# Kernel tuning notes

Hardware: AMD Instinct MI355X
Metric: run time of the kernel (lower is better)

Reference implementation:

```python
import jax, jax.numpy as jnp
import numpy as np

N_NODES = 50000
N_EDGES = 800000
D_IN = 64
D_OUT = 64
N_REL = 8


def setup_inputs() -> dict:
    key = jax.random.key(0)
    ks = jax.random.split(key, 7)
    x = jax.random.normal(ks[0], (N_NODES, D_IN), jnp.float32)
    src = jax.random.randint(ks[1], (N_EDGES,), 0, N_NODES)   # neighbor ids
    dst = jax.random.randint(ks[2], (N_EDGES,), 0, N_NODES)   # center node ids
    rel = jax.random.randint(ks[3], (N_EDGES,), 0, N_REL)
    # xavier_uniform for W_r: [R, 2*d, d]
    lim = float(np.sqrt(6.0 / (2 * D_IN + D_IN)))
    W_r = jax.random.uniform(ks[4], (N_REL, 2 * D_IN, D_IN), jnp.float32, -lim, lim)
    # nn.Linear(2*d, d_out): weight [d_out, 2*d], bias [d_out]
    lim2 = float(1.0 / np.sqrt(2 * D_IN))
    W_lin = jax.random.uniform(ks[5], (D_OUT, 2 * D_IN), jnp.float32, -lim2, lim2)
    b_lin = jax.random.uniform(ks[6], (D_OUT,), jnp.float32, -lim2, lim2)
    return {"x": x, "src": src, "dst": dst, "rel": rel,
            "W_r": W_r, "W_lin": W_lin, "b_lin": b_lin}


def reference(x, src, dst, rel, W_r, W_lin, b_lin):
    n, d = x.shape
    e = src.shape[0]
    # gate logit per edge: (concat(x[dst], x[src]) @ W_r[rel]).sum(-1)
    # == concat(x[dst], x[src]) . W_r[rel].sum(-1)  -- mathematically identical,
    # avoids materializing the [E, 2d, d] matmul the torch loop performs.
    w = W_r.sum(-1)                      # [R, 2d]
    w_dst, w_src = w[:, :d], w[:, d:]    # [R, d] each
    logit = jnp.sum(x[dst] * w_dst[rel], axis=-1) + jnp.sum(x[src] * w_src[rel], axis=-1)  # [E]
    gate = jax.nn.sigmoid(logit)[:, None]        # [E, 1]
    weighted = x[src] * gate                     # [E, d]
    # scatter-mean over destination nodes (nodes with no edges stay zero)
    agg_sum = jax.ops.segment_sum(weighted, dst, num_segments=n)            # [N, d]
    cnt = jax.ops.segment_sum(jnp.ones((e,), x.dtype), dst, num_segments=n)  # [N]
    agg = agg_sum / jnp.maximum(cnt, 1.0)[:, None]
    combined = jnp.concatenate([x, agg], axis=-1)  # [N, 2d]
    out = combined @ W_lin.T + b_lin               # [N, d_out]
    return jax.nn.leaky_relu(out, negative_slope=0.01)
```

## Files before the change

### kernel.cpp

```cpp
#include <hip/hip_runtime.h>
#include <hip/hip_fp16.h>
#include <cmath>

#define N_NODES 50000
#define N_EDGES 800000
#define D 64
#define N_REL 8

#define NODES_PER_BLK 32
#define TN 16
#define MAXDEG 64
#define NSEG 8
#define SEG_DIV 6250

static __device__ __forceinline__ unsigned f2bf(float f) {
    unsigned u = __float_as_uint(f);
    return (u + 0x7FFFu + ((u >> 16) & 1u)) >> 16;
}
#define BFLO(u) __uint_as_float((u) << 16)
#define BFHI(u) __uint_as_float((u) & 0xFFFF0000u)

__global__ void wprep_kernel(const float* __restrict__ W_r, float* __restrict__ w,
                             int* __restrict__ cnt) {
    int t = blockIdx.x * blockDim.x + threadIdx.x;
    if (t < N_REL * 2 * D) {
        const float* p = W_r + (size_t)t * D;
        float s = 0.0f;
#pragma unroll
        for (int k = 0; k < D; ++k) s += p[k];
        w[t] = s;
    }
    for (int i = t; i < N_NODES; i += gridDim.x * blockDim.x)
        cnt[i] = 0;
}

__global__ __launch_bounds__(256) void tables_kernel(
    const float* __restrict__ x, const float* __restrict__ w,
    float* __restrict__ Dn, float* __restrict__ Sr,
    unsigned short* __restrict__ xb)
{
    __shared__ float xs[TN][68];
    __shared__ float ws[16][68];

    int tid = threadIdx.x;
    int n0  = blockIdx.x * TN;

    for (int i = tid; i < 16 * 64; i += 256)
        ws[i >> 6][i & 63] = w[i];
    for (int i = tid; i < TN * 64; i += 256) {
        int n = n0 + (i >> 6);
        xs[i >> 6][i & 63] = (n < N_NODES) ? x[(size_t)n * D + (i & 63)] : 0.f;
    }
    __syncthreads();

    for (int i = tid; i < TN * 64; i += 256) {
        int n = n0 + (i >> 6);
        if (n < N_NODES) xb[(size_t)n0 * D + i] = (unsigned short)f2bf(xs[i >> 6][i & 63]);
    }

    int q = tid & 15, nl = tid >> 4;
    float acc = 0.f;
#pragma unroll
    for (int k = 0; k < 64; k += 4) {
        float4 a = *(const float4*)&xs[nl][k];
        float4 b = *(const float4*)&ws[q][k];
        acc += a.x * b.x + a.y * b.y + a.z * b.z + a.w * b.w;
    }
    int n = n0 + nl;
    if (n < N_NODES) {
        int r = q >> 1;
        if ((q & 1) == 0) Dn[n * 8 + r] = acc;
        else              Sr[n * 8 + r] = acc;
    }
}

__global__ __launch_bounds__(256) void scatter_kernel(
    const int* __restrict__ src, const int* __restrict__ dst,
    const int* __restrict__ rel,
    int* __restrict__ cnt,
    const float* __restrict__ Dn, const float* __restrict__ Sr,
    unsigned int* __restrict__ epack) {
    int seg   = blockIdx.x & (NSEG - 1);
    int chunk = blockIdx.x >> 3;
    int e = chunk * 256 + threadIdx.x;
    if (e >= N_EDGES) return;

    int d = dst[e];
    int s = src[e];
    int r = rel[e];
    asm volatile("" :: "v"(d), "v"(s), "v"(r));

    if ((unsigned)d / SEG_DIV != (unsigned)seg) return;

    int rank = atomicAdd(&cnt[d], 1);

    float logit = Dn[d * 8 + r] + Sr[s * 8 + r];
    float gate = 1.0f / (1.0f + __expf(-logit));
    if (rank < MAXDEG) {
        unsigned pv = ((unsigned)__half_as_ushort(__float2half_rn(gate)) << 16)
                    | (unsigned)s;
        epack[(size_t)d * MAXDEG + rank] = pv;
    }
}

__global__ __launch_bounds__(256) void agg_kernel(
    const unsigned short* __restrict__ xb,
    const int*   __restrict__ cnt,
    const unsigned int* __restrict__ epack,
    unsigned int* __restrict__ aggb)
{
    int n    = (blockIdx.x * blockDim.x + threadIdx.x) >> 6;
    int lane = threadIdx.x & 63;
    if (n >= N_NODES) return;

    int deg = cnt[n];
    int m   = (deg < MAXDEG) ? deg : MAXDEG;

    unsigned ev = 0u;
    if (lane < m) ev = epack[(size_t)n * MAXDEG + lane];
    float gl = __half2float(__ushort_as_half((unsigned short)(ev >> 16)));
    int   ol = (int)(ev & 0xFFFFu) * D;

    int sub = lane >> 4;
    int q4  = (lane & 15) * 4;

    float ax = 0.f, ay = 0.f, az = 0.f, aw = 0.f;

    for (int base = 0; base < m; base += 8) {
        int e0 = base + sub;
        int e1 = base + 4 + sub;
        float g0 = __shfl(gl, e0, 64);
        int   o0 = __shfl(ol, e0, 64);
        float g1 = __shfl(gl, e1, 64);
        int   o1 = __shfl(ol, e1, 64);
        uint2 u0 = *(const uint2*)&xb[(size_t)o0 + q4];
        uint2 u1 = *(const uint2*)&xb[(size_t)o1 + q4];
        ax += g0 * BFLO(u0.x) + g1 * BFLO(u1.x);
        ay += g0 * BFHI(u0.x) + g1 * BFHI(u1.x);
        az += g0 * BFLO(u0.y) + g1 * BFLO(u1.y);
        aw += g0 * BFHI(u0.y) + g1 * BFHI(u1.y);
    }

#pragma unroll
    for (int off = 16; off <= 32; off <<= 1) {
        ax += __shfl_xor(ax, off, 64);
        ay += __shfl_xor(ay, off, 64);
        az += __shfl_xor(az, off, 64);
        aw += __shfl_xor(aw, off, 64);
    }

    if (sub == 0) {
        float inv = 1.0f / fmaxf((float)deg, 1.0f);
        uint2 pr;
        pr.x = f2bf(ax * inv) | (f2bf(ay * inv) << 16);
        pr.y = f2bf(az * inv) | (f2bf(aw * inv) << 16);
        *(uint2*)&aggb[(size_t)n * 32 + 2 * (lane & 15)] = pr;
    }
}

__global__ __launch_bounds__(256, 6) void lin_kernel(
    const unsigned int* __restrict__ xbu,
    const unsigned int* __restrict__ aggb,
    const float* __restrict__ W_lin,
    const float* __restrict__ b_lin,
    float* __restrict__ out)
{
    __shared__ unsigned int W2[64][66];
    __shared__ unsigned int c2[NODES_PER_BLK][66];
    __shared__ float b_lds[64];

    int tid = threadIdx.x;
    int n0  = blockIdx.x * NODES_PER_BLK;

    for (int i = tid; i < 64 * 64; i += 256) {
        int j = i >> 6, kp = i & 63;
        float2 wv = *(const float2*)&W_lin[j * 128 + kp * 2];
        W2[j][kp] = f2bf(wv.x) | (f2bf(wv.y) << 16);
    }
    if (tid < 64) b_lds[tid] = b_lin[tid];

    for (int i = tid; i < NODES_PER_BLK * 32; i += 256) {
        int nl = i >> 5, kp = i & 31;
        int n  = n0 + nl;
        unsigned vx = 0u, va = 0u;
        if (n < N_NODES) {
            vx = xbu[(size_t)n * 32 + kp];
            va = aggb[(size_t)n * 32 + kp];
        }
        c2[nl][kp]      = vx;
        c2[nl][32 + kp] = va;
    }
    __syncthreads();

    int tx = tid & 15, ty = tid >> 4;
    float acc[2][4];
#pragma unroll
    for (int i = 0; i < 2; ++i)
#pragma unroll
        for (int jj = 0; jj < 4; ++jj) acc[i][jj] = b_lds[tx + 16 * jj];

#pragma unroll 2
    for (int kp = 0; kp < 64; kp += 2) {
        uint2 cu[2], wu[4];
        cu[0] = *(const uint2*)&c2[ty][kp];
        cu[1] = *(const uint2*)&c2[ty + 16][kp];
#pragma unroll
        for (int jj = 0; jj < 4; ++jj)
            wu[jj] = *(const uint2*)&W2[tx + 16 * jj][kp];
#pragma unroll
        for (int i = 0; i < 2; ++i) {
            float cx = BFLO(cu[i].x), cy = BFHI(cu[i].x);
            float cz = BFLO(cu[i].y), cw = BFHI(cu[i].y);
#pragma unroll
            for (int jj = 0; jj < 4; ++jj) {
                acc[i][jj] += cx * BFLO(wu[jj].x) + cy * BFHI(wu[jj].x)
                            + cz * BFLO(wu[jj].y) + cw * BFHI(wu[jj].y);
            }
        }
    }

#pragma unroll
    for (int i = 0; i < 2; ++i) {
        int n = n0 + ty + 16 * i;
        if (n < N_NODES) {
#pragma unroll
            for (int jj = 0; jj < 4; ++jj) {
                float v = acc[i][jj];
                out[(size_t)n * D + tx + 16 * jj] = (v > 0.f) ? v : 0.01f * v;
            }
        }
    }
}

extern "C" void kernel_launch(void* const* d_in, const int* in_sizes, int n_in,
                              void* d_out, int out_size, void* d_ws, size_t ws_size,
                              hipStream_t stream) {
    const float* x     = (const float*)d_in[0];
    const int*   src   = (const int*)  d_in[1];
    const int*   dst   = (const int*)  d_in[2];
    const int*   rel   = (const int*)  d_in[3];
    const float* W_r   = (const float*)d_in[4];
    const float* W_lin = (const float*)d_in[5];
    const float* b_lin = (const float*)d_in[6];
    float* out = (float*)d_out;

    char* p = (char*)d_ws;
    float*  w       = (float*)p;                p += 4096;
    float*  Dn      = (float*)p;                p += (size_t)N_NODES * 8 * 4;
    float*  Sr      = (float*)p;                p += (size_t)N_NODES * 8 * 4;
    int*    cnt     = (int*)p;                  p += 256 * 1024;
    unsigned int* epack = (unsigned int*)p;     p += (size_t)N_NODES * MAXDEG * 4;
    unsigned short* xb = (unsigned short*)p;    p += (size_t)N_NODES * D * 2;
    unsigned int* aggb = (unsigned int*)p;      p += (size_t)N_NODES * 32 * 4;

    wprep_kernel<<<512, 256, 0, stream>>>(W_r, w, cnt);
    tables_kernel<<<(N_NODES + TN - 1) / TN, 256, 0, stream>>>(x, w, Dn, Sr, xb);
    scatter_kernel<<<NSEG * ((N_EDGES + 255) / 256), 256, 0, stream>>>(
        src, dst, rel, cnt, Dn, Sr, epack);
    agg_kernel<<<(N_NODES * 64 + 255) / 256, 256, 0, stream>>>(xb, cnt, epack, aggb);
    lin_kernel<<<(N_NODES + NODES_PER_BLK - 1) / NODES_PER_BLK, 256, 0, stream>>>(
        (const unsigned int*)xb, aggb, W_lin, b_lin, out);
}
```

Measured before the change: 176.3 us.

## Split scatter into gate pass plus segment-bucketed compaction and placement pass

```diff
diff --git a/kernel.cpp b/kernel.cpp
--- a/kernel.cpp
+++ b/kernel.cpp
@@ -12,6 +12,7 @@
 #define MAXDEG 64
 #define NSEG 8
 #define SEG_DIV 6250
+#define SEG_STRIDE 112640
 
 static __device__ __forceinline__ unsigned f2bf(float f) {
     unsigned u = __float_as_uint(f);
@@ -21,7 +22,7 @@
 #define BFHI(u) __uint_as_float((u) & 0xFFFF0000u)
 
 __global__ void wprep_kernel(const float* __restrict__ W_r, float* __restrict__ w,
-                             int* __restrict__ cnt) {
+                             int* __restrict__ cnt, int* __restrict__ segCnt) {
     int t = blockIdx.x * blockDim.x + threadIdx.x;
     if (t < N_REL * 2 * D) {
         const float* p = W_r + (size_t)t * D;
@@ -30,6 +31,7 @@
         for (int k = 0; k < D; ++k) s += p[k];
         w[t] = s;
     }
+    if (t < 128) segCnt[t] = 0;
     for (int i = t; i < N_NODES; i += gridDim.x * blockDim.x)
         cnt[i] = 0;
 }
@@ -74,33 +76,60 @@
     }
 }
 
-__global__ __launch_bounds__(256) void scatter_kernel(
+__global__ __launch_bounds__(256) void gate_kernel(
     const int* __restrict__ src, const int* __restrict__ dst,
     const int* __restrict__ rel,
-    int* __restrict__ cnt,
+    int* __restrict__ cnt, int* __restrict__ segCnt,
     const float* __restrict__ Dn, const float* __restrict__ Sr,
-    unsigned int* __restrict__ epack) {
-    int seg   = blockIdx.x & (NSEG - 1);
-    int chunk = blockIdx.x >> 3;
-    int e = chunk * 256 + threadIdx.x;
-    if (e >= N_EDGES) return;
+    uint2* __restrict__ compact)
+{
+    int e    = blockIdx.x * 256 + threadIdx.x;
+    int lane = threadIdx.x & 63;
 
     int d = dst[e];
     int s = src[e];
     int r = rel[e];
     asm volatile("" :: "v"(d), "v"(s), "v"(r));
 
-    if ((unsigned)d / SEG_DIV != (unsigned)seg) return;
-
     int rank = atomicAdd(&cnt[d], 1);
 
     float logit = Dn[d * 8 + r] + Sr[s * 8 + r];
     float gate = 1.0f / (1.0f + __expf(-logit));
-    if (rank < MAXDEG) {
-        unsigned pv = ((unsigned)__half_as_ushort(__float2half_rn(gate)) << 16)
-                    | (unsigned)s;
-        epack[(size_t)d * MAXDEG + rank] = pv;
-    }
+
+    uint2 rec;
+    rec.x = ((unsigned)__half_as_ushort(__float2half_rn(gate)) << 16) | (unsigned)s;
+    rec.y = ((unsigned)rank << 16) | (unsigned)d;
+
+    unsigned seg = (unsigned)d / SEG_DIV;
+
+#pragma unroll
+    for (int k = 0; k < NSEG; ++k) {
+        unsigned long long m = __ballot(seg == (unsigned)k);
+        if (seg == (unsigned)k) {
+            int pop    = __popcll(m);
+            int before = __popcll(m & ((1ull << lane) - 1ull));
+            int leader = (int)__ffsll((long long)m) - 1;
+            int base = 0;
+            if (lane == leader) base = atomicAdd(&segCnt[k * 16], pop);
+            base = __shfl(base, leader, 64);
+            compact[(size_t)k * SEG_STRIDE + base + before] = rec;
+        }
+    }
+}
+
+__global__ __launch_bounds__(256) void place_kernel(
+    const int* __restrict__ segCnt, const uint2* __restrict__ compact,
+    unsigned int* __restrict__ epack)
+{
+    int seg   = blockIdx.x & (NSEG - 1);
+    int chunk = blockIdx.x >> 3;
+    int i = chunk * 256 + threadIdx.x;
+    if (i >= segCnt[seg * 16]) return;
+    uint2 rec = compact[(size_t)seg * SEG_STRIDE + i];
+    int d    = (int)(rec.y & 0xFFFFu);
+    int rank = (int)(rec.y >> 16);
+    if (rank < MAXDEG)
+        epack[(size_t)d * MAXDEG + rank] = rec.x;
 }
 
 __global__ __launch_bounds__(256) void agg_kernel(
@@ -249,14 +278,18 @@
     float*  Dn      = (float*)p;                p += (size_t)N_NODES * 8 * 4;
     float*  Sr      = (float*)p;                p += (size_t)N_NODES * 8 * 4;
     int*    cnt     = (int*)p;                  p += 256 * 1024;
+    int*    segCnt  = (int*)p;                  p += 4096;
+    uint2*  compact = (uint2*)p;                p += (size_t)NSEG * SEG_STRIDE * 8;
     unsigned int* epack = (unsigned int*)p;     p += (size_t)N_NODES * MAXDEG * 4;
     unsigned short* xb = (unsigned short*)p;    p += (size_t)N_NODES * D * 2;
     unsigned int* aggb = (unsigned int*)p;      p += (size_t)N_NODES * 32 * 4;
 
-    wprep_kernel<<<512, 256, 0, stream>>>(W_r, w, cnt);
+    wprep_kernel<<<512, 256, 0, stream>>>(W_r, w, cnt, segCnt);
     tables_kernel<<<(N_NODES + TN - 1) / TN, 256, 0, stream>>>(x, w, Dn, Sr, xb);
-    scatter_kernel<<<NSEG * ((N_EDGES + 255) / 256), 256, 0, stream>>>(
-        src, dst, rel, cnt, Dn, Sr, epack);
+    gate_kernel<<<N_EDGES / 256, 256, 0, stream>>>(
+        src, dst, rel, cnt, segCnt, Dn, Sr, compact);
+    place_kernel<<<NSEG * (SEG_STRIDE / 256), 256, 0, stream>>>(
+        segCnt, compact, epack);
     agg_kernel<<<(N_NODES * 64 + 255) / 256, 256, 0, stream>>>(xb, cnt, epack, aggb);
     lin_kernel<<<(N_NODES + NODES_PER_BLK - 1) / NODES_PER_BLK, 256, 0, stream>>>(
         (const unsigned int*)xb, aggb, W_lin, b_lin, out);
```

After: 505.3 us. +186.6%, slower.

## Split edge scatter into linear gate pass and segmented placement pass

Applied to the files above, without the earlier changes.

```diff
diff --git a/kernel.cpp b/kernel.cpp
--- a/kernel.cpp
+++ b/kernel.cpp
@@ -74,33 +74,45 @@
     }
 }
 
-__global__ __launch_bounds__(256) void scatter_kernel(
+__global__ __launch_bounds__(256) void gate_kernel(
     const int* __restrict__ src, const int* __restrict__ dst,
     const int* __restrict__ rel,
     int* __restrict__ cnt,
     const float* __restrict__ Dn, const float* __restrict__ Sr,
-    unsigned int* __restrict__ epack) {
-    int seg   = blockIdx.x & (NSEG - 1);
-    int chunk = blockIdx.x >> 3;
-    int e = chunk * 256 + threadIdx.x;
-    if (e >= N_EDGES) return;
+    uint2* __restrict__ erec)
+{
+    int e = blockIdx.x * 256 + threadIdx.x;
 
     int d = dst[e];
     int s = src[e];
     int r = rel[e];
     asm volatile("" :: "v"(d), "v"(s), "v"(r));
 
-    if ((unsigned)d / SEG_DIV != (unsigned)seg) return;
-
     int rank = atomicAdd(&cnt[d], 1);
 
     float logit = Dn[d * 8 + r] + Sr[s * 8 + r];
     float gate = 1.0f / (1.0f + __expf(-logit));
-    if (rank < MAXDEG) {
-        unsigned pv = ((unsigned)__half_as_ushort(__float2half_rn(gate)) << 16)
-                    | (unsigned)s;
-        epack[(size_t)d * MAXDEG + rank] = pv;
-    }
+
+    uint2 rec;
+    rec.x = ((unsigned)__half_as_ushort(__float2half_rn(gate)) << 16) | (unsigned)s;
+    rec.y = ((unsigned)rank << 16) | (unsigned)d;
+    erec[e] = rec;
+}
+
+__global__ __launch_bounds__(256) void place_kernel(
+    const uint2* __restrict__ erec,
+    unsigned int* __restrict__ epack)
+{
+    int seg   = blockIdx.x & (NSEG - 1);
+    int chunk = blockIdx.x >> 3;
+    int e = chunk * 256 + threadIdx.x;
+
+    uint2 rec = erec[e];
+    int d = (int)(rec.y & 0xFFFFu);
+    if ((unsigned)d / SEG_DIV != (unsigned)seg) return;
+    int rank = (int)(rec.y >> 16);
+    if (rank < MAXDEG)
+        epack[(size_t)d * MAXDEG + rank] = rec.x;
 }
 
 __global__ __launch_bounds__(256) void agg_kernel(
@@ -249,14 +261,16 @@
     float*  Dn      = (float*)p;                p += (size_t)N_NODES * 8 * 4;
     float*  Sr      = (float*)p;                p += (size_t)N_NODES * 8 * 4;
     int*    cnt     = (int*)p;                  p += 256 * 1024;
+    uint2*  erec    = (uint2*)p;                p += (size_t)N_EDGES * 8;
     unsigned int* epack = (unsigned int*)p;     p += (size_t)N_NODES * MAXDEG * 4;
     unsigned short* xb = (unsigned short*)p;    p += (size_t)N_NODES * D * 2;
     unsigned int* aggb = (unsigned int*)p;      p += (size_t)N_NODES * 32 * 4;
 
     wprep_kernel<<<512, 256, 0, stream>>>(W_r, w, cnt);
     tables_kernel<<<(N_NODES + TN - 1) / TN, 256, 0, stream>>>(x, w, Dn, Sr, xb);
-    scatter_kernel<<<NSEG * ((N_EDGES + 255) / 256), 256, 0, stream>>>(
-        src, dst, rel, cnt, Dn, Sr, epack);
+    gate_kernel<<<N_EDGES / 256, 256, 0, stream>>>(
+        src, dst, rel, cnt, Dn, Sr, erec);
+    place_kernel<<<NSEG * (N_EDGES / 256), 256, 0, stream>>>(erec, epack);
     agg_kernel<<<(N_NODES * 64 + 255) / 256, 256, 0, stream>>>(xb, cnt, epack, aggb);
     lin_kernel<<<(N_NODES + NODES_PER_BLK - 1) / NODES_PER_BLK, 256, 0, stream>>>(
         (const unsigned int*)xb, aggb, W_lin, b_lin, out);
```

Result: slower. 188.0 us (+6.6%).

## Fuse gather-aggregation into linear kernel, writing aggregates directly to shared memory

Applied to the files above, without the earlier changes.

```diff
diff --git a/kernel.cpp b/kernel.cpp
--- a/kernel.cpp
+++ b/kernel.cpp
@@ -103,64 +103,11 @@
     }
 }
 
-__global__ __launch_bounds__(256) void agg_kernel(
+__global__ __launch_bounds__(256) void agglin_kernel(
     const unsigned short* __restrict__ xb,
+    const unsigned int* __restrict__ xbu,
     const int*   __restrict__ cnt,
     const unsigned int* __restrict__ epack,
-    unsigned int* __restrict__ aggb)
-{
-    int n    = (blockIdx.x * blockDim.x + threadIdx.x) >> 6;
-    int lane = threadIdx.x & 63;
-    if (n >= N_NODES) return;
-
-    int deg = cnt[n];
-    int m   = (deg < MAXDEG) ? deg : MAXDEG;
-
-    unsigned ev = 0u;
-    if (lane < m) ev = epack[(size_t)n * MAXDEG + lane];
-    float gl = __half2float(__ushort_as_half((unsigned short)(ev >> 16)));
-    int   ol = (int)(ev & 0xFFFFu) * D;
-
-    int sub = lane >> 4;
-    int q4  = (lane & 15) * 4;
-
-    float ax = 0.f, ay = 0.f, az = 0.f, aw = 0.f;
-
-    for (int base = 0; base < m; base += 8) {
-        int e0 = base + sub;
-        int e1 = base + 4 + sub;
-        float g0 = __shfl(gl, e0, 64);
-        int   o0 = __shfl(ol, e0, 64);
-        float g1 = __shfl(gl, e1, 64);
-        int   o1 = __shfl(ol, e1, 64);
-        uint2 u0 = *(const uint2*)&xb[(size_t)o0 + q4];
-        uint2 u1 = *(const uint2*)&xb[(size_t)o1 + q4];
-        ax += g0 * BFLO(u0.x) + g1 * BFLO(u1.x);
-        ay += g0 * BFHI(u0.x) + g1 * BFHI(u1.x);
-        az += g0 * BFLO(u0.y) + g1 * BFLO(u1.y);
-        aw += g0 * BFHI(u0.y) + g1 * BFHI(u1.y);
-    }
-
-#pragma unroll
-    for (int off = 16; off <= 32; off <<= 1) {
-        ax += __shfl_xor(ax, off, 64);
-        ay += __shfl_xor(ay, off, 64);
-        az += __shfl_xor(az, off, 64);
-        aw += __shfl_xor(aw, off, 64);
-    }
-
-    if (sub == 0) {
-        float inv = 1.0f / fmaxf((float)deg, 1.0f);
-        uint2 pr;
-        pr.x = f2bf(ax * inv) | (f2bf(ay * inv) << 16);
-        pr.y = f2bf(az * inv) | (f2bf(aw * inv) << 16);
-        *(uint2*)&aggb[(size_t)n * 32 + 2 * (lane & 15)] = pr;
-    }
-}
-
-__global__ __launch_bounds__(256, 6) void lin_kernel(
-    const unsigned int* __restrict__ xbu,
-    const unsigned int* __restrict__ aggb,
     const float* __restrict__ W_lin,
     const float* __restrict__ b_lin,
     float* __restrict__ out)
@@ -169,26 +116,80 @@
     __shared__ unsigned int c2[NODES_PER_BLK][66];
     __shared__ float b_lds[64];
 
-    int tid = threadIdx.x;
-    int n0  = blockIdx.x * NODES_PER_BLK;
+    int tid  = threadIdx.x;
+    int n0   = blockIdx.x * NODES_PER_BLK;
+    int lane = tid & 63;
+    int wv   = tid >> 6;
 
     for (int i = tid; i < 64 * 64; i += 256) {
         int j = i >> 6, kp = i & 63;
-        float2 wv = *(const float2*)&W_lin[j * 128 + kp * 2];
-        W2[j][kp] = f2bf(wv.x) | (f2bf(wv.y) << 16);
+        float2 wvv = *(const float2*)&W_lin[j * 128 + kp * 2];
+        W2[j][kp] = f2bf(wvv.x) | (f2bf(wvv.y) << 16);
     }
     if (tid < 64) b_lds[tid] = b_lin[tid];
 
     for (int i = tid; i < NODES_PER_BLK * 32; i += 256) {
         int nl = i >> 5, kp = i & 31;
         int n  = n0 + nl;
-        unsigned vx = 0u, va = 0u;
-        if (n < N_NODES) {
-            vx = xbu[(size_t)n * 32 + kp];
-            va = aggb[(size_t)n * 32 + kp];
-        }
-        c2[nl][kp]      = vx;
-        c2[nl][32 + kp] = va;
+        c2[nl][kp] = (n < N_NODES) ? xbu[(size_t)n * 32 + kp] : 0u;
+    }
+
+    int nbase = n0 + wv * 8;
+
+    int      degv[8];
+    unsigned ev[8];
+#pragma unroll
+    for (int i = 0; i < 8; ++i) {
+        int n = nbase + i;
+        degv[i] = (n < N_NODES) ? cnt[n] : 0;
+    }
+#pragma unroll
+    for (int i = 0; i < 8; ++i) {
+        int n = nbase + i;
+        ev[i] = (n < N_NODES) ? epack[(size_t)n * MAXDEG + lane] : 0u;
+    }
+
+    int sub = lane >> 4;
+    int q   = lane & 15;
+    int q4  = q * 4;
+
+#pragma unroll
+    for (int i = 0; i < 8; ++i) {
+        int m = (degv[i] < MAXDEG) ? degv[i] : MAXDEG;
+        unsigned e_m = (lane < m) ? ev[i] : 0u;
+        float gl = __half2float(__ushort_as_half((unsigned short)(e_m >> 16)));
+        int   ol = (int)(e_m & 0xFFFFu) * D;
+
+        float ax = 0.f, ay = 0.f, az = 0.f, aw = 0.f;
+        for (int base = 0; base < m; base += 8) {
+            int e0 = base + sub;
+            int e1 = base + 4 + sub;
+            float g0 = __shfl(gl, e0, 64);
+            int   o0 = __shfl(ol, e0, 64);
+            float g1 = __shfl(gl, e1, 64);
+            int   o1 = __shfl(ol, e1, 64);
+            uint2 u0 = *(const uint2*)&xb[(size_t)o0 + q4];
+            uint2 u1 = *(const uint2*)&xb[(size_t)o1 + q4];
+            ax += g0 * BFLO(u0.x) + g1 * BFLO(u1.x);
+            ay += g0 * BFHI(u0.x) + g1 * BFHI(u1.x);
+            az += g0 * BFLO(u0.y) + g1 * BFLO(u1.y);
+            aw += g0 * BFHI(u0.y) + g1 * BFHI(u1.y);
+        }
+
+#pragma unroll
+        for (int off = 16; off <= 32; off <<= 1) {
+            ax += __shfl_xor(ax, off, 64);
+            ay += __shfl_xor(ay, off, 64);
+            az += __shfl_xor(az, off, 64);
+            aw += __shfl_xor(aw, off, 64);
+        }
+
+        if (sub == 0) {
+            float inv = 1.0f / fmaxf((float)degv[i], 1.0f);
+            int nl = wv * 8 + i;
+            c2[nl][32 + 2 * q]     = f2bf(ax * inv) | (f2bf(ay * inv) << 16);
+            c2[nl][32 + 2 * q + 1] = f2bf(az * inv) | (f2bf(aw * inv) << 16);
+        }
     }
     __syncthreads();
 
@@ -251,13 +252,11 @@
     int*    cnt     = (int*)p;                  p += 256 * 1024;
     unsigned int* epack = (unsigned int*)p;     p += (size_t)N_NODES * MAXDEG * 4;
     unsigned short* xb = (unsigned short*)p;    p += (size_t)N_NODES * D * 2;
-    unsigned int* aggb = (unsigned int*)p;      p += (size_t)N_NODES * 32 * 4;
 
     wprep_kernel<<<512, 256, 0, stream>>>(W_r, w, cnt);
     tables_kernel<<<(N_NODES + TN - 1) / TN, 256, 0, stream>>>(x, w, Dn, Sr, xb);
     scatter_kernel<<<NSEG * ((N_EDGES + 255) / 256), 256, 0, stream>>>(
         src, dst, rel, cnt, Dn, Sr, epack);
-    agg_kernel<<<(N_NODES * 64 + 255) / 256, 256, 0, stream>>>(xb, cnt, epack, aggb);
-    lin_kernel<<<(N_NODES + NODES_PER_BLK - 1) / NODES_PER_BLK, 256, 0, stream>>>(
-        (const unsigned int*)xb, aggb, W_lin, b_lin, out);
-}
+    agglin_kernel<<<(N_NODES + NODES_PER_BLK - 1) / NODES_PER_BLK, 256, 0, stream>>>(
+        xb, (const unsigned int*)xb, cnt, epack, W_lin, b_lin, out);
+}
```

After: 177.4 us. About the same (+0.6%).
